# Kernel tuning notes

Measured on AMD Instinct MI355X. Metric: run time of the kernel, lower is better.

The kernel has to match this reference:

```python
import jax, jax.numpy as jnp
import numpy as np
import math

N = 50000   # nodes
E = 800000  # edges
D = 64      # in_feat_dim == out_feat_dim
T = 8       # num node types
R = 8       # num relations
SQRT_DK = math.sqrt(D)


def typed_matmul(x, W, types, num_types):
    """Row-wise x[i] @ W[types[i]] without materializing [E, D, D] gathered weights."""
    out = jnp.zeros((x.shape[0], W.shape[-1]), x.dtype)
    for t in range(num_types):
        out = out + jnp.where((types == t)[:, None], x @ W[t], 0.0)
    return out


def segment_softmax(score, index, num_segments):
    smax = jax.ops.segment_max(score, index, num_segments=num_segments)
    ex = jnp.exp(score - smax[index])
    ssum = jax.ops.segment_sum(ex, index, num_segments=num_segments)
    return ex / (ssum[index] + 1e-16)


def setup_inputs() -> dict:
    key = jax.random.key(0)
    ks = jax.random.split(key, 10)
    h = jax.random.normal(ks[0], (N, D), dtype=jnp.float32)
    adj = jax.random.randint(ks[1], (2, E), 0, N, dtype=jnp.int64)
    edge_type = jax.random.randint(ks[2], (E,), 0, R, dtype=jnp.int64)
    node_type = jax.random.randint(ks[3], (N,), 0, T, dtype=jnp.int64)
    k_weights = jax.random.uniform(ks[4], (T, D, D), dtype=jnp.float32)
    q_weights = jax.random.uniform(ks[5], (T, D, D), dtype=jnp.float32)
    v_weights = jax.random.uniform(ks[6], (T, D, D), dtype=jnp.float32)
    a_weights = jax.random.uniform(ks[7], (T, D, D), dtype=jnp.float32)
    relation_att = jax.random.uniform(ks[8], (R, D, D), dtype=jnp.float32)
    relation_msg = jax.random.uniform(ks[9], (R, D, D), dtype=jnp.float32)
    relation_pri = jnp.ones((R, 1), dtype=jnp.float32)
    skip = jnp.ones((T,), dtype=jnp.float32)
    return {
        "h": h, "adj": adj, "edge_type": edge_type, "node_type": node_type,
        "src_type": 0, "dst_type": 0,
        "k_weights": k_weights, "q_weights": q_weights, "v_weights": v_weights,
        "a_weights": a_weights, "relation_pri": relation_pri,
        "relation_att": relation_att, "relation_msg": relation_msg, "skip": skip,
    }


def reference(h, adj, edge_type, node_type, src_type, dst_type,
              k_weights, q_weights, v_weights, a_weights,
              relation_pri, relation_att, relation_msg, skip):
    src = adj[0]  # _j side (messages come from src)
    dst = adj[1]  # _i side (scatter/softmax index)

    # Node-type-indexed projections (done per node, then gathered per edge --
    # identical math to the per-edge bmm in the original).
    k_node = typed_matmul(h, k_weights, node_type, T)  # [N, D]
    q_node = typed_matmul(h, q_weights, node_type, T)
    v_node = typed_matmul(h, v_weights, node_type, T)

    # Relation-indexed per-edge transforms.
    k = typed_matmul(k_node[src], relation_att, edge_type, R)  # [E, D]
    v = typed_matmul(v_node[src], relation_msg, edge_type, R)  # [E, D]
    q = q_node[dst]                                            # [E, D]

    attn_score = jnp.sum(k * q, axis=1, keepdims=True) * relation_pri[edge_type] / SQRT_DK  # [E, 1]
    alpha = segment_softmax(attn_score, dst, N)  # edge softmax over incoming edges
    rst = v * alpha                              # [E, D]

    agg = jax.ops.segment_sum(rst, dst, num_segments=N)  # [N, D]

    # Update: node-type-indexed output transform scaled by sigmoid(skip[type]).
    trans_out = typed_matmul(agg, a_weights, node_type, T)
    alpha_skip = jax.nn.sigmoid(skip[node_type])
    return trans_out * alpha_skip[:, None]
```

## Files before the change

kernel.cpp:

```cpp
#include <hip/hip_runtime.h>
#include <math.h>

typedef float f32x4 __attribute__((ext_vector_type(4)));
typedef short bf16x8 __attribute__((ext_vector_type(8)));
typedef _Float16 f16x8 __attribute__((ext_vector_type(8)));
typedef _Float16 f16x4 __attribute__((ext_vector_type(4)));

#define D 64
#define TT 8
#define RR 8

#define SCAN_TPB 256
#define SCAN_CH 4
#define SCAN_ELEMS (SCAN_TPB * SCAN_CH)

#define HIST_CH 8
#define SCAT_CH 4
#define SCORE_XB 256
#define V2_XB 64
#define AGG_XB 512

__device__ __forceinline__ float bf2f(unsigned short u) {
    union { unsigned int i; float f; } x;
    x.i = ((unsigned int)u) << 16;
    return x.f;
}
__device__ __forceinline__ unsigned short f2bf(float f) {
    union { float f; unsigned int i; } x;
    x.f = f;
    unsigned int i = x.i;
    unsigned int r = (i + 0x7FFFu + ((i >> 16) & 1u)) >> 16;
    return (unsigned short)r;
}
struct BfPair { short hi; short lo; };
__device__ __forceinline__ BfPair split2(float x) {
    BfPair p;
    unsigned short h = f2bf(x);
    p.hi = (short)h;
    p.lo = (short)f2bf(x - bf2f(h));
    return p;
}
__device__ __forceinline__ void load_A_split(const float* __restrict__ p, bf16x8& ah, bf16x8& al) {
#pragma unroll
    for (int i = 0; i < 8; ++i) {
        BfPair s = split2(p[i]);
        ah[i] = s.hi; al[i] = s.lo;
    }
}
__device__ __forceinline__ void load_B_split(const float* __restrict__ W, int ks, int c, int lane,
                                             bf16x8& bh, bf16x8& bl) {
    int n = lane & 15, q = lane >> 4;
#pragma unroll
    for (int i = 0; i < 8; ++i) {
        BfPair s = split2(W[(ks * 32 + q * 8 + i) * 64 + c * 16 + n]);
        bh[i] = s.hi; bl[i] = s.lo;
    }
}
__device__ __forceinline__ void load_B_split_f16(const float* __restrict__ W, int ks, int c, int lane,
                                                 f16x8& bh, f16x8& bl) {
    int n = lane & 15, q = lane >> 4;
#pragma unroll
    for (int i = 0; i < 8; ++i) {
        float w = W[(ks * 32 + q * 8 + i) * 64 + c * 16 + n];
        _Float16 h = (_Float16)w;
        bh[i] = h;
        bl[i] = (_Float16)(w - (float)h);
    }
}
__device__ __forceinline__ f16x8 load_B_frag_f16(const float* __restrict__ W, int ks, int c, int lane) {
    int n = lane & 15, q = lane >> 4;
    f16x8 r;
#pragma unroll
    for (int i = 0; i < 8; ++i)
        r[i] = (_Float16)W[(ks * 32 + q * 8 + i) * 64 + c * 16 + n];
    return r;
}

#define MFMA16(a, b, c) __builtin_amdgcn_mfma_f32_16x16x32_bf16(a, b, c, 0, 0, 0)
#define MFMAH(a, b, c)  __builtin_amdgcn_mfma_f32_16x16x32_f16(a, b, c, 0, 0, 0)

#define SPLIT_MFMA_BODY(acc, A0h, A0l, A1h, A1l, Bh, Bl)          \
    _Pragma("unroll")                                             \
    for (int c = 0; c < 4; ++c) {                                 \
        acc[c] = MFMA16(A0h, Bh[0][c], acc[c]);                   \
        acc[c] = MFMA16(A0l, Bh[0][c], acc[c]);                   \
        acc[c] = MFMA16(A0h, Bl[0][c], acc[c]);                   \
        acc[c] = MFMA16(A1h, Bh[1][c], acc[c]);                   \
        acc[c] = MFMA16(A1l, Bh[1][c], acc[c]);                   \
        acc[c] = MFMA16(A1h, Bl[1][c], acc[c]);                   \
    }

__global__ void hist_kernel(const int* __restrict__ dst, const int* __restrict__ et,
                            const int* __restrict__ nt,
                            int* __restrict__ deg, int* __restrict__ tcnt, int* __restrict__ rcnt,
                            int* __restrict__ erank, int N, int E) {
    __shared__ int l_r[RR], l_t[TT];
    if (threadIdx.x < RR) l_r[threadIdx.x] = 0;
    if (threadIdx.x < TT) l_t[threadIdx.x] = 0;
    __syncthreads();
    const int stride = gridDim.x * blockDim.x;
    const int tid = blockIdx.x * blockDim.x + threadIdx.x;
#pragma unroll
    for (int i = 0; i < HIST_CH; ++i) {
        int e = tid + i * stride;
        if (e < E) {
            erank[e] = atomicAdd(&deg[dst[e]], 1);
            atomicAdd(&l_r[et[e]], 1);
        }
    }
#pragma unroll
    for (int i = 0; i < HIST_CH; ++i) {
        int n = tid + i * stride;
        if (n < N) atomicAdd(&l_t[nt[n]], 1);
    }
    __syncthreads();
    if (threadIdx.x < RR && l_r[threadIdx.x]) atomicAdd(&rcnt[threadIdx.x], l_r[threadIdx.x]);
    if (threadIdx.x < TT && l_t[threadIdx.x]) atomicAdd(&tcnt[threadIdx.x], l_t[threadIdx.x]);
}

__global__ void scan_sum_kernel(const int* __restrict__ deg, int* __restrict__ bsum, int N) {
    __shared__ int ws[SCAN_TPB / 64];
    int tid = threadIdx.x;
    int base = blockIdx.x * SCAN_ELEMS + tid * SCAN_CH;
    int s = 0;
#pragma unroll
    for (int i = 0; i < SCAN_CH; ++i) {
        int idx = base + i;
        if (idx < N) s += deg[idx];
    }
#pragma unroll
    for (int d = 32; d; d >>= 1) s += __shfl_xor(s, d, 64);
    if ((tid & 63) == 0) ws[tid >> 6] = s;
    __syncthreads();
    if (tid == 0) {
        int t = 0;
#pragma unroll
        for (int i = 0; i < SCAN_TPB / 64; ++i) t += ws[i];
        bsum[blockIdx.x] = t;
    }
}
__global__ void scan_out_kernel(const int* __restrict__ deg, const int* __restrict__ bsum, int nsb,
                                int* __restrict__ off, int N, int Etot,
                                const int* __restrict__ tcnt, int* __restrict__ toff, int* __restrict__ tcur,
                                const int* __restrict__ rcnt, int* __restrict__ roff, int* __restrict__ rcur) {
    __shared__ int ts[SCAN_TPB];
    __shared__ int bb;
    int tid = threadIdx.x;
    if (tid < 64) {
        int v = 0;
        if (nsb <= 64) {
            v = (tid < nsb && tid < blockIdx.x) ? bsum[tid] : 0;
#pragma unroll
            for (int d = 32; d; d >>= 1) v += __shfl_xor(v, d, 64);
        } else if (tid == 0) {
            for (int b = 0; b < blockIdx.x; ++b) v += bsum[b];
        }
        if (tid == 0) bb = v;
    }
    if (blockIdx.x == 0 && tid == 1) {
        int a = 0;
        for (int t = 0; t < TT; ++t) { toff[t] = a; tcur[t] = a; a += tcnt[t]; }
        toff[TT] = a;
        int b2 = 0;
        for (int r = 0; r < RR; ++r) { roff[r] = b2; rcur[r] = b2; b2 += rcnt[r]; }
        roff[RR] = b2;
        off[N] = Etot;
    }
    int base = blockIdx.x * SCAN_ELEMS + tid * SCAN_CH;
    int loc[SCAN_CH];
    int s = 0;
#pragma unroll
    for (int i = 0; i < SCAN_CH; ++i) {
        int idx = base + i;
        int v = (idx < N) ? deg[idx] : 0;
        loc[i] = v; s += v;
    }
    ts[tid] = s;
    __syncthreads();
    for (int sh = 1; sh < SCAN_TPB; sh <<= 1) {
        int v = (tid >= sh) ? ts[tid - sh] : 0;
        __syncthreads();
        ts[tid] += v;
        __syncthreads();
    }
    int run = bb + ((tid > 0) ? ts[tid - 1] : 0);
#pragma unroll
    for (int i = 0; i < SCAN_CH; ++i) {
        int idx = base + i;
        if (idx < N) { off[idx] = run; run += loc[i]; }
    }
}

__global__ void scatter_kernel(const int* __restrict__ src, const int* __restrict__ dst,
                               const int* __restrict__ et, const int* __restrict__ nt,
                               const int* __restrict__ offs, const int* __restrict__ erank,
                               int* __restrict__ tcur, int* __restrict__ rcur,
                               int* __restrict__ rsrc, int* __restrict__ rdst,
                               int* __restrict__ rdpos, int* __restrict__ nidx, int N, int E) {
    __shared__ int l_r[RR], l_t[TT], base_r[RR], base_t[TT];
    if (threadIdx.x < RR) l_r[threadIdx.x] = 0;
    if (threadIdx.x < TT) l_t[threadIdx.x] = 0;
    __syncthreads();
    const int stride = gridDim.x * blockDim.x;
    const int tid = blockIdx.x * blockDim.x + threadIdx.x;
    int s[SCAT_CH], d[SCAT_CH], r[SCAT_CH], rrank[SCAT_CH];
    int t[SCAT_CH], trank[SCAT_CH];
#pragma unroll
    for (int i = 0; i < SCAT_CH; ++i) {
        int e = tid + i * stride;
        if (e < E) {
            s[i] = src[e]; d[i] = dst[e]; r[i] = et[e];
            rrank[i] = atomicAdd(&l_r[r[i]], 1);
        }
        int n = tid + i * stride;
        if (n < N) {
            t[i] = nt[n];
            trank[i] = atomicAdd(&l_t[t[i]], 1);
        }
    }
    __syncthreads();
    if (threadIdx.x < RR)
        base_r[threadIdx.x] = l_r[threadIdx.x] ? atomicAdd(&rcur[threadIdx.x], l_r[threadIdx.x]) : 0;
    if (threadIdx.x < TT)
        base_t[threadIdx.x] = l_t[threadIdx.x] ? atomicAdd(&tcur[threadIdx.x], l_t[threadIdx.x]) : 0;
    __syncthreads();
#pragma unroll
    for (int i = 0; i < SCAT_CH; ++i) {
        int e = tid + i * stride;
        if (e < E) {
            int pos = offs[d[i]] + erank[e];
            int rp = base_r[r[i]] + rrank[i];
            rsrc[rp] = s[i]; rdst[rp] = d[i]; rdpos[rp] = pos;
        }
        int n = tid + i * stride;
        if (n < N) nidx[base_t[t[i]] + trank[i]] = n;
    }
}

__global__ void proj_kernel(const float* __restrict__ h,
                            const float* __restrict__ Wk, const float* __restrict__ Wq,
                            const float* __restrict__ Wv,
                            const int* __restrict__ toff, const int* __restrict__ nidx,
                            _Float16* __restrict__ kh16,
                            _Float16* __restrict__ qout, _Float16* __restrict__ vout) {
    const int t = blockIdx.z, a = blockIdx.y, lane = threadIdx.x;
    const int beg = toff[t], end = toff[t + 1], cnt = end - beg;
    if (cnt <= 0) return;
    const int nstrips = (cnt + 15) >> 4;
    const float* W = (a == 0 ? Wk : (a == 1 ? Wq : Wv)) + (size_t)t * 4096;
    const int m = lane & 15, quad = lane >> 4;

    bf16x8 Bh[2][4], Bl[2][4];
#pragma unroll
    for (int ks = 0; ks < 2; ++ks)
#pragma unroll
        for (int c = 0; c < 4; ++c) load_B_split(W, ks, c, lane, Bh[ks][c], Bl[ks][c]);

    _Float16* out = (a == 0) ? kh16 : (a == 1 ? qout : vout);

    for (int s = blockIdx.x; s < nstrips; s += gridDim.x) {
        int base = beg + s * 16;
        int rA = base + m; if (rA > end - 1) rA = end - 1;
        const float* hp = h + (size_t)nidx[rA] * D;
        bf16x8 A0h, A0l, A1h, A1l;
        load_A_split(hp + quad * 8, A0h, A0l);
        load_A_split(hp + 32 + quad * 8, A1h, A1l);
        f32x4 acc[4];
#pragma unroll
        for (int c = 0; c < 4; ++c) acc[c] = (f32x4){0.f, 0.f, 0.f, 0.f};
        SPLIT_MFMA_BODY(acc, A0h, A0l, A1h, A1l, Bh, Bl)
#pragma unroll
        for (int reg = 0; reg < 4; ++reg) {
            int rr = base + quad * 4 + reg;
            if (rr < end) {
                int nid = nidx[rr];
#pragma unroll
                for (int c = 0; c < 4; ++c)
                    out[(size_t)nid * D + c * 16 + m] = (_Float16)acc[c][reg];
            }
        }
    }
}

__global__ void score_v2_kernel(const int* __restrict__ rsrc, const int* __restrict__ rdst,
                                const int* __restrict__ rdpos, const int* __restrict__ roff,
                                const _Float16* __restrict__ kh16,
                                const _Float16* __restrict__ qn, const float* __restrict__ Aatt,
                                const float* __restrict__ pri, int2* __restrict__ rec,
                                const _Float16* __restrict__ vn, const float* __restrict__ Amsg,
                                _Float16* __restrict__ V2, int N) {
    const int r = blockIdx.y;
    const int lane = threadIdx.x & 63;
    const int wv = threadIdx.x >> 6;
    const int m = lane & 15, quad = lane >> 4;

    if (blockIdx.x >= SCORE_XB) {
        const int g = (blockIdx.x - SCORE_XB) * 4 + wv;
        const int nstrips = (N + 15) >> 4;
        const float* W = Amsg + (size_t)r * 4096;
        f16x8 B[2][4];
#pragma unroll
        for (int ks = 0; ks < 2; ++ks)
#pragma unroll
            for (int c = 0; c < 4; ++c) B[ks][c] = load_B_frag_f16(W, ks, c, lane);

        for (int s = g; s < nstrips; s += V2_XB * 4) {
            int base = s * 16;
            int rA = base + m; if (rA > N - 1) rA = N - 1;
            f16x8 A0 = *(const f16x8*)(vn + (size_t)rA * D + quad * 8);
            f16x8 A1 = *(const f16x8*)(vn + (size_t)rA * D + 32 + quad * 8);
            f32x4 acc[4];
#pragma unroll
            for (int c = 0; c < 4; ++c) acc[c] = (f32x4){0.f, 0.f, 0.f, 0.f};
#pragma unroll
            for (int c = 0; c < 4; ++c) {
                acc[c] = MFMAH(A0, B[0][c], acc[c]);
                acc[c] = MFMAH(A1, B[1][c], acc[c]);
            }
#pragma unroll
            for (int reg = 0; reg < 4; ++reg) {
                int rr = base + quad * 4 + reg;
                if (rr < N) {
#pragma unroll
                    for (int c = 0; c < 4; ++c)
                        V2[((size_t)rr * RR + r) * D + c * 16 + m] = (_Float16)acc[c][reg];
                }
            }
        }
        return;
    }

    const int beg = roff[r], end = roff[r + 1], cnt = end - beg;
    if (cnt <= 0) return;
    const int nstrips = (cnt + 15) >> 4;
    const float scale = pri[r] * 0.125f;
    const float* W = Aatt + (size_t)r * 4096;

    f16x8 Bh[2][4], Bl[2][4];
#pragma unroll
    for (int ks = 0; ks < 2; ++ks)
#pragma unroll
        for (int c = 0; c < 4; ++c) load_B_split_f16(W, ks, c, lane, Bh[ks][c], Bl[ks][c]);

    const int g = blockIdx.x * 4 + wv;
    for (int st = g; st < nstrips; st += SCORE_XB * 4) {
        int base = st * 16;
        int ia = base + m; if (ia > cnt - 1) ia = cnt - 1;
        int s = rsrc[beg + ia];
        const _Float16* kr = kh16 + (size_t)s * D;
        f16x8 A0 = *(const f16x8*)(kr + quad * 8);
        f16x8 A1 = *(const f16x8*)(kr + 32 + quad * 8);
        f32x4 acc[4];
#pragma unroll
        for (int c = 0; c < 4; ++c) acc[c] = (f32x4){0.f, 0.f, 0.f, 0.f};
#pragma unroll
        for (int c = 0; c < 4; ++c) {
            acc[c] = MFMAH(A0, Bh[0][c], acc[c]);
            acc[c] = MFMAH(A0, Bl[0][c], acc[c]);
            acc[c] = MFMAH(A1, Bh[1][c], acc[c]);
            acc[c] = MFMAH(A1, Bl[1][c], acc[c]);
        }

        float p4[4];
#pragma unroll
        for (int reg = 0; reg < 4; ++reg) {
            int ie = base + quad * 4 + reg; if (ie > cnt - 1) ie = cnt - 1;
            const _Float16* qp = qn + (size_t)rdst[beg + ie] * D + m;
            float pr = acc[0][reg] * (float)qp[0] + acc[1][reg] * (float)qp[16]
                     + acc[2][reg] * (float)qp[32] + acc[3][reg] * (float)qp[48];
#pragma unroll
            for (int d = 8; d; d >>= 1) pr += __shfl_xor(pr, d, 64);
            p4[reg] = pr;
        }
        if (m < 4) {
            int idx = base + quad * 4 + m;
            if (idx < cnt) {
                float v = (m == 0) ? p4[0] : (m == 1) ? p4[1] : (m == 2) ? p4[2] : p4[3];
                int sagain = rsrc[beg + idx];
                int2 rc;
                rc.x = __float_as_int(v * scale);
                rc.y = (sagain << 3) | r;
                rec[rdpos[beg + idx]] = rc;
            }
        }
    }
}

__global__ void agg_out_kernel(const int* __restrict__ offs, const int2* __restrict__ rec,
                               const _Float16* __restrict__ V2,
                               const float* __restrict__ Wa, const float* __restrict__ skp,
                               const int* __restrict__ toff, const int* __restrict__ nidx,
                               float* __restrict__ out) {
    const int t = blockIdx.y;
    const int beg = toff[t], end = toff[t + 1], cnt = end - beg;
    if (cnt <= 0) return;
    const int nstrips = (cnt + 15) >> 4;
    const int lane = threadIdx.x & 63;
    const int wv = threadIdx.x >> 6;
    const int quad = lane >> 4, ql = lane & 15;
    const int q16 = wv * 4 + quad;
    const int qb = quad << 4;
    const int m = lane & 15, qd = lane >> 4;
    const float sg = 1.f / (1.f + __expf(-skp[t]));

    __shared__ float As[16][68];

    bf16x8 Bh2[2], Bl2[2];
    const float* W = Wa + (size_t)t * 4096;
#pragma unroll
    for (int ks = 0; ks < 2; ++ks) load_B_split(W, ks, wv, lane, Bh2[ks], Bl2[ks]);

    for (int s = blockIdx.x; s < nstrips; s += gridDim.x) {
        int base = beg + s * 16;
        int rr = base + q16; if (rr > end - 1) rr = end - 1;
        int i = nidx[rr];
        const int ebeg = offs[i], eend = offs[i + 1];
        float mmax = -INFINITY, lsum = 0.f;
        float a0 = 0.f, a1 = 0.f, a2 = 0.f, a3 = 0.f;
        for (int cs = ebeg; cs < eend; cs += 16) {
            int cl = eend - cs; if (cl > 16) cl = 16;
            int2 rc; rc.y = 0;
            float sc = -INFINITY;
            if (ql < cl) { rc = rec[cs + ql]; sc = __int_as_float(rc.x); }
            float cm = sc;
#pragma unroll
            for (int d = 8; d; d >>= 1) cm = fmaxf(cm, __shfl_xor(cm, d, 64));
            float mn = fmaxf(mmax, cm);
            float cf = __expf(mmax - mn);
            float ex = (ql < cl) ? __expf(sc - mn) : 0.f;
            float csum = ex;
#pragma unroll
            for (int d = 8; d; d >>= 1) csum += __shfl_xor(csum, d, 64);
            lsum = lsum * cf + csum;
            a0 *= cf; a1 *= cf; a2 *= cf; a3 *= cf;
            for (int e = 0; e < cl; e += 4) {
                float w0 = __shfl(ex, qb + e, 64),     w1 = __shfl(ex, qb + e + 1, 64);
                float w2 = __shfl(ex, qb + e + 2, 64), w3 = __shfl(ex, qb + e + 3, 64);
                int   i0 = __shfl(rc.y, qb + e, 64),     i1 = __shfl(rc.y, qb + e + 1, 64);
                int   i2 = __shfl(rc.y, qb + e + 2, 64), i3 = __shfl(rc.y, qb + e + 3, 64);
                f16x4 v0 = *(const f16x4*)(V2 + (size_t)i0 * D + ql * 4);
                f16x4 v1 = *(const f16x4*)(V2 + (size_t)i1 * D + ql * 4);
                f16x4 v2 = *(const f16x4*)(V2 + (size_t)i2 * D + ql * 4);
                f16x4 v3 = *(const f16x4*)(V2 + (size_t)i3 * D + ql * 4);
                a0 += w0 * (float)v0[0] + w1 * (float)v1[0] + w2 * (float)v2[0] + w3 * (float)v3[0];
                a1 += w0 * (float)v0[1] + w1 * (float)v1[1] + w2 * (float)v2[1] + w3 * (float)v3[1];
                a2 += w0 * (float)v0[2] + w1 * (float)v1[2] + w2 * (float)v2[2] + w3 * (float)v3[2];
                a3 += w0 * (float)v0[3] + w1 * (float)v1[3] + w2 * (float)v2[3] + w3 * (float)v3[3];
            }
            mmax = mn;
        }
        float inv = 1.f / (lsum + 1e-16f);
        As[q16][ql * 4 + 0] = a0 * inv;
        As[q16][ql * 4 + 1] = a1 * inv;
        As[q16][ql * 4 + 2] = a2 * inv;
        As[q16][ql * 4 + 3] = a3 * inv;
        __syncthreads();

        bf16x8 A0h, A0l, A1h, A1l;
        load_A_split(&As[m][qd * 8], A0h, A0l);
        load_A_split(&As[m][32 + qd * 8], A1h, A1l);
        f32x4 acc = (f32x4){0.f, 0.f, 0.f, 0.f};
        acc = MFMA16(A0h, Bh2[0], acc);
        acc = MFMA16(A0l, Bh2[0], acc);
        acc = MFMA16(A0h, Bl2[0], acc);
        acc = MFMA16(A1h, Bh2[1], acc);
        acc = MFMA16(A1l, Bh2[1], acc);
        acc = MFMA16(A1h, Bl2[1], acc);
#pragma unroll
        for (int reg = 0; reg < 4; ++reg) {
            int rrr = base + qd * 4 + reg;
            if (rrr < end)
                out[(size_t)nidx[rrr] * D + wv * 16 + m] = acc[reg] * sg;
        }
        __syncthreads();
    }
}

extern "C" void kernel_launch(void* const* d_in, const int* in_sizes, int n_in,
                              void* d_out, int out_size, void* d_ws, size_t ws_size,
                              hipStream_t stream) {
    const float* h     = (const float*)d_in[0];
    const int*   adj   = (const int*)d_in[1];
    const int*   etype = (const int*)d_in[2];
    const int*   ntype = (const int*)d_in[3];
    const float* Wk    = (const float*)d_in[6];
    const float* Wq    = (const float*)d_in[7];
    const float* Wv    = (const float*)d_in[8];
    const float* Wa    = (const float*)d_in[9];
    const float* pri   = (const float*)d_in[10];
    const float* Aatt  = (const float*)d_in[11];
    const float* Amsg  = (const float*)d_in[12];
    const float* skp   = (const float*)d_in[13];
    const int N = in_sizes[3];
    const int E = in_sizes[2];
    float* out = (float*)d_out;

    char* w = (char*)d_ws;
    auto alloc = [&](size_t b) { char* p = w; w += (b + 255) & ~(size_t)255; return p; };
    _Float16* kh16 = (_Float16*)alloc((size_t)N * D * 2);
    _Float16* qn   = (_Float16*)alloc((size_t)N * D * 2);
    _Float16* vn   = (_Float16*)alloc((size_t)N * D * 2);
    _Float16* V2   = (_Float16*)alloc((size_t)N * RR * D * 2);
    int* deg  = (int*)alloc((size_t)(N + 16) * 4);
    int* tcnt = deg + N;
    int* rcnt = deg + N + 8;
    int* offs = (int*)alloc((size_t)(N + 1) * 4);
    int* erank = (int*)alloc((size_t)E * 4);
    int* toff = (int*)alloc(64);
    int* tcur = (int*)alloc(64);
    int* roff = (int*)alloc(64);
    int* rcur = (int*)alloc(64);
    int2* rec = (int2*)alloc((size_t)E * 8);
    int* rsrc  = (int*)alloc((size_t)E * 4);
    int* rdst  = (int*)alloc((size_t)E * 4);
    int* rdpos = (int*)alloc((size_t)E * 4);
    int* nidx  = (int*)alloc((size_t)N * 4);
    const int nsb = (N + SCAN_ELEMS - 1) / SCAN_ELEMS;
    int* bsum  = (int*)alloc((size_t)nsb * 4);

    (void)hipMemsetAsync(deg, 0, (size_t)(N + 16) * 4, stream);

    const int mx = (E > N ? E : N);
    const int histBlocks = (mx + 256 * HIST_CH - 1) / (256 * HIST_CH);
    hist_kernel<<<histBlocks, 256, 0, stream>>>(adj + E, etype, ntype, deg, tcnt, rcnt, erank, N, E);
    scan_sum_kernel<<<nsb, SCAN_TPB, 0, stream>>>(deg, bsum, N);
    scan_out_kernel<<<nsb, SCAN_TPB, 0, stream>>>(deg, bsum, nsb, offs, N, E,
                                                  tcnt, toff, tcur, rcnt, roff, rcur);
    const int scatBlocks = (mx + 256 * SCAT_CH - 1) / (256 * SCAT_CH);
    scatter_kernel<<<scatBlocks, 256, 0, stream>>>(adj, adj + E, etype, ntype,
                                                   offs, erank, tcur, rcur,
                                                   rsrc, rdst, rdpos, nidx, N, E);
    proj_kernel<<<dim3(128, 3, TT), 64, 0, stream>>>(h, Wk, Wq, Wv, toff, nidx, kh16, qn, vn);
    score_v2_kernel<<<dim3(SCORE_XB + V2_XB, RR), 256, 0, stream>>>(rsrc, rdst, rdpos, roff,
                                                                    kh16, qn, Aatt, pri, rec,
                                                                    vn, Amsg, V2, N);
    agg_out_kernel<<<dim3(AGG_XB, TT), 256, 0, stream>>>(offs, rec, V2, Wa, skp, toff, nidx, out);
}
```

Measured before the change: 258.0 us.

## Fuse CSR build stages into one cooperative kernel with grid syncs

Replaces the memset, histogram, two scan kernels and scatter kernel with a single cooperative build kernel that separates the phases with grid-wide syncs. Per-edge data (packed src/relation, dst, rank) stays in registers between phases, so the erank buffer and the re-reads of src, dst and edge type go away. This is meant to cut several launch gaps and some global traffic, at the cost of four grid barriers. The kernel also assumes the fixed grid covers all edges (8 per thread) and all nodes (one per thread), so it only works for sizes within that limit.

```diff
diff --git a/kernel.cpp b/kernel.cpp
--- a/kernel.cpp
+++ b/kernel.cpp
@@ -1,5 +1,8 @@
 #include <hip/hip_runtime.h>
+#include <hip/hip_cooperative_groups.h>
 #include <math.h>
+
+namespace cg = cooperative_groups;
 
 typedef float f32x4 __attribute__((ext_vector_type(4)));
 typedef short bf16x8 __attribute__((ext_vector_type(8)));
@@ -14,8 +17,8 @@
 #define SCAN_CH 4
 #define SCAN_ELEMS (SCAN_TPB * SCAN_CH)
 
-#define HIST_CH 8
-#define SCAT_CH 4
+#define BUILD_XB 512
+#define BUILD_EPT 8
 #define SCORE_XB 256
 #define V2_XB 64
 #define AGG_XB 512
@@ -90,151 +93,141 @@
         acc[c] = MFMA16(A1h, Bl[1][c], acc[c]);                   \
     }
 
-__global__ void hist_kernel(const int* __restrict__ dst, const int* __restrict__ et,
-                            const int* __restrict__ nt,
-                            int* __restrict__ deg, int* __restrict__ tcnt, int* __restrict__ rcnt,
-                            int* __restrict__ erank, int N, int E) {
-    __shared__ int l_r[RR], l_t[TT];
+__global__ void build_kernel(const int* __restrict__ src, const int* __restrict__ dst,
+                             const int* __restrict__ et, const int* __restrict__ nt,
+                             int* __restrict__ deg,
+                             int* __restrict__ offs,
+                             int* __restrict__ toff, int* __restrict__ tcur,
+                             int* __restrict__ roff, int* __restrict__ rcur,
+                             int* __restrict__ rsrc, int* __restrict__ rdst,
+                             int* __restrict__ rdpos, int* __restrict__ nidx,
+                             int* __restrict__ bsum, int nsb, int N, int E) {
+    cg::grid_group grid = cg::this_grid();
+    const int tid = blockIdx.x * blockDim.x + threadIdx.x;
+    const int nth = gridDim.x * blockDim.x;
+    int* tcnt = deg + N;
+    int* rcnt = deg + N + 8;
+
+    __shared__ int l_r[RR], l_t[TT], base_r[RR], base_t[TT];
+    __shared__ int ts[SCAN_TPB];
+    __shared__ int ws[SCAN_TPB / 64];
+    __shared__ int bbs;
+
+    for (int i = tid; i < N + 16; i += nth) deg[i] = 0;
     if (threadIdx.x < RR) l_r[threadIdx.x] = 0;
     if (threadIdx.x < TT) l_t[threadIdx.x] = 0;
-    __syncthreads();
-    const int stride = gridDim.x * blockDim.x;
-    const int tid = blockIdx.x * blockDim.x + threadIdx.x;
-#pragma unroll
-    for (int i = 0; i < HIST_CH; ++i) {
-        int e = tid + i * stride;
+    grid.sync();
+
+    int epk[BUILD_EPT], ed[BUILD_EPT], erk[BUILD_EPT], rrk[BUILD_EPT];
+#pragma unroll
+    for (int i = 0; i < BUILD_EPT; ++i) {
+        int e = tid + i * nth;
         if (e < E) {
-            erank[e] = atomicAdd(&deg[dst[e]], 1);
-            atomicAdd(&l_r[et[e]], 1);
-        }
-    }
-#pragma unroll
-    for (int i = 0; i < HIST_CH; ++i) {
-        int n = tid + i * stride;
-        if (n < N) atomicAdd(&l_t[nt[n]], 1);
+            int s = src[e], d = dst[e], r = et[e];
+            epk[i] = (s << 3) | r;
+            ed[i] = d;
+            erk[i] = atomicAdd(&deg[d], 1);
+            rrk[i] = atomicAdd(&l_r[r], 1);
+        }
+    }
+    int myt = 0, mytrank = 0;
+    if (tid < N) {
+        myt = nt[tid];
+        mytrank = atomicAdd(&l_t[myt], 1);
     }
     __syncthreads();
     if (threadIdx.x < RR && l_r[threadIdx.x]) atomicAdd(&rcnt[threadIdx.x], l_r[threadIdx.x]);
     if (threadIdx.x < TT && l_t[threadIdx.x]) atomicAdd(&tcnt[threadIdx.x], l_t[threadIdx.x]);
-}
-
-__global__ void scan_sum_kernel(const int* __restrict__ deg, int* __restrict__ bsum, int N) {
-    __shared__ int ws[SCAN_TPB / 64];
-    int tid = threadIdx.x;
-    int base = blockIdx.x * SCAN_ELEMS + tid * SCAN_CH;
-    int s = 0;
-#pragma unroll
-    for (int i = 0; i < SCAN_CH; ++i) {
-        int idx = base + i;
-        if (idx < N) s += deg[idx];
-    }
-#pragma unroll
-    for (int d = 32; d; d >>= 1) s += __shfl_xor(s, d, 64);
-    if ((tid & 63) == 0) ws[tid >> 6] = s;
-    __syncthreads();
-    if (tid == 0) {
-        int t = 0;
-#pragma unroll
-        for (int i = 0; i < SCAN_TPB / 64; ++i) t += ws[i];
-        bsum[blockIdx.x] = t;
-    }
-}
-__global__ void scan_out_kernel(const int* __restrict__ deg, const int* __restrict__ bsum, int nsb,
-                                int* __restrict__ off, int N, int Etot,
-                                const int* __restrict__ tcnt, int* __restrict__ toff, int* __restrict__ tcur,
-                                const int* __restrict__ rcnt, int* __restrict__ roff, int* __restrict__ rcur) {
-    __shared__ int ts[SCAN_TPB];
-    __shared__ int bb;
-    int tid = threadIdx.x;
-    if (tid < 64) {
-        int v = 0;
-        if (nsb <= 64) {
-            v = (tid < nsb && tid < blockIdx.x) ? bsum[tid] : 0;
-#pragma unroll
-            for (int d = 32; d; d >>= 1) v += __shfl_xor(v, d, 64);
-        } else if (tid == 0) {
-            for (int b = 0; b < blockIdx.x; ++b) v += bsum[b];
-        }
-        if (tid == 0) bb = v;
-    }
-    if (blockIdx.x == 0 && tid == 1) {
-        int a = 0;
-        for (int t = 0; t < TT; ++t) { toff[t] = a; tcur[t] = a; a += tcnt[t]; }
-        toff[TT] = a;
-        int b2 = 0;
-        for (int r = 0; r < RR; ++r) { roff[r] = b2; rcur[r] = b2; b2 += rcnt[r]; }
-        roff[RR] = b2;
-        off[N] = Etot;
-    }
-    int base = blockIdx.x * SCAN_ELEMS + tid * SCAN_CH;
-    int loc[SCAN_CH];
-    int s = 0;
-#pragma unroll
-    for (int i = 0; i < SCAN_CH; ++i) {
-        int idx = base + i;
-        int v = (idx < N) ? deg[idx] : 0;
-        loc[i] = v; s += v;
-    }
-    ts[tid] = s;
-    __syncthreads();
-    for (int sh = 1; sh < SCAN_TPB; sh <<= 1) {
-        int v = (tid >= sh) ? ts[tid - sh] : 0;
+    grid.sync();
+
+    if (blockIdx.x < nsb) {
+        int t0 = threadIdx.x;
+        int base = blockIdx.x * SCAN_ELEMS + t0 * SCAN_CH;
+        int s = 0;
+#pragma unroll
+        for (int i = 0; i < SCAN_CH; ++i) {
+            int idx = base + i;
+            if (idx < N) s += deg[idx];
+        }
+#pragma unroll
+        for (int d = 32; d; d >>= 1) s += __shfl_xor(s, d, 64);
+        if ((t0 & 63) == 0) ws[t0 >> 6] = s;
         __syncthreads();
-        ts[tid] += v;
+        if (t0 == 0) {
+            int t = 0;
+#pragma unroll
+            for (int i = 0; i < SCAN_TPB / 64; ++i) t += ws[i];
+            bsum[blockIdx.x] = t;
+        }
+    }
+    grid.sync();
+
+    if (blockIdx.x < nsb) {
+        int t0 = threadIdx.x;
+        if (t0 < 64) {
+            int v = 0;
+            if (nsb <= 64) {
+                v = (t0 < nsb && t0 < blockIdx.x) ? bsum[t0] : 0;
+#pragma unroll
+                for (int d = 32; d; d >>= 1) v += __shfl_xor(v, d, 64);
+            } else if (t0 == 0) {
+                for (int b = 0; b < blockIdx.x; ++b) v += bsum[b];
+            }
+            if (t0 == 0) bbs = v;
+        }
+        if (blockIdx.x == 0 && t0 == 1) {
+            int a = 0;
+            for (int t = 0; t < TT; ++t) { toff[t] = a; tcur[t] = a; a += tcnt[t]; }
+            toff[TT] = a;
+            int b2 = 0;
+            for (int r = 0; r < RR; ++r) { roff[r] = b2; rcur[r] = b2; b2 += rcnt[r]; }
+            roff[RR] = b2;
+            offs[N] = E;
+        }
+        int base = blockIdx.x * SCAN_ELEMS + t0 * SCAN_CH;
+        int loc[SCAN_CH];
+        int s = 0;
+#pragma unroll
+        for (int i = 0; i < SCAN_CH; ++i) {
+            int idx = base + i;
+            int v = (idx < N) ? deg[idx] : 0;
+            loc[i] = v; s += v;
+        }
+        ts[t0] = s;
         __syncthreads();
-    }
-    int run = bb + ((tid > 0) ? ts[tid - 1] : 0);
-#pragma unroll
-    for (int i = 0; i < SCAN_CH; ++i) {
-        int idx = base + i;
-        if (idx < N) { off[idx] = run; run += loc[i]; }
-    }
-}
-
-__global__ void scatter_kernel(const int* __restrict__ src, const int* __restrict__ dst,
-                               const int* __restrict__ et, const int* __restrict__ nt,
-                               const int* __restrict__ offs, const int* __restrict__ erank,
-                               int* __restrict__ tcur, int* __restrict__ rcur,
-                               int* __restrict__ rsrc, int* __restrict__ rdst,
-                               int* __restrict__ rdpos, int* __restrict__ nidx, int N, int E) {
-    __shared__ int l_r[RR], l_t[TT], base_r[RR], base_t[TT];
-    if (threadIdx.x < RR) l_r[threadIdx.x] = 0;
-    if (threadIdx.x < TT) l_t[threadIdx.x] = 0;
-    __syncthreads();
-    const int stride = gridDim.x * blockDim.x;
-    const int tid = blockIdx.x * blockDim.x + threadIdx.x;
-    int s[SCAT_CH], d[SCAT_CH], r[SCAT_CH], rrank[SCAT_CH];
-    int t[SCAT_CH], trank[SCAT_CH];
-#pragma unroll
-    for (int i = 0; i < SCAT_CH; ++i) {
-        int e = tid + i * stride;
-        if (e < E) {
-            s[i] = src[e]; d[i] = dst[e]; r[i] = et[e];
-            rrank[i] = atomicAdd(&l_r[r[i]], 1);
-        }
-        int n = tid + i * stride;
-        if (n < N) {
-            t[i] = nt[n];
-            trank[i] = atomicAdd(&l_t[t[i]], 1);
-        }
-    }
-    __syncthreads();
+        for (int sh = 1; sh < SCAN_TPB; sh <<= 1) {
+            int v = (t0 >= sh) ? ts[t0 - sh] : 0;
+            __syncthreads();
+            ts[t0] += v;
+            __syncthreads();
+        }
+        int run = bbs + ((t0 > 0) ? ts[t0 - 1] : 0);
+#pragma unroll
+        for (int i = 0; i < SCAN_CH; ++i) {
+            int idx = base + i;
+            if (idx < N) { offs[idx] = run; run += loc[i]; }
+        }
+    }
+    grid.sync();
+
     if (threadIdx.x < RR)
         base_r[threadIdx.x] = l_r[threadIdx.x] ? atomicAdd(&rcur[threadIdx.x], l_r[threadIdx.x]) : 0;
     if (threadIdx.x < TT)
         base_t[threadIdx.x] = l_t[threadIdx.x] ? atomicAdd(&tcur[threadIdx.x], l_t[threadIdx.x]) : 0;
     __syncthreads();
 #pragma unroll
-    for (int i = 0; i < SCAT_CH; ++i) {
-        int e = tid + i * stride;
+    for (int i = 0; i < BUILD_EPT; ++i) {
+        int e = tid + i * nth;
         if (e < E) {
-            int pos = offs[d[i]] + erank[e];
-            int rp = base_r[r[i]] + rrank[i];
-            rsrc[rp] = s[i]; rdst[rp] = d[i]; rdpos[rp] = pos;
-        }
-        int n = tid + i * stride;
-        if (n < N) nidx[base_t[t[i]] + trank[i]] = n;
-    }
+            int r = epk[i] & 7;
+            int pos = offs[ed[i]] + erk[i];
+            int rp = base_r[r] + rrk[i];
+            rsrc[rp] = epk[i] >> 3;
+            rdst[rp] = ed[i];
+            rdpos[rp] = pos;
+        }
+    }
+    if (tid < N) nidx[base_t[myt] + mytrank] = tid;
 }
 
 __global__ void proj_kernel(const float* __restrict__ h,
@@ -502,10 +495,7 @@
     _Float16* vn   = (_Float16*)alloc((size_t)N * D * 2);
     _Float16* V2   = (_Float16*)alloc((size_t)N * RR * D * 2);
     int* deg  = (int*)alloc((size_t)(N + 16) * 4);
-    int* tcnt = deg + N;
-    int* rcnt = deg + N + 8;
     int* offs = (int*)alloc((size_t)(N + 1) * 4);
-    int* erank = (int*)alloc((size_t)E * 4);
     int* toff = (int*)alloc(64);
     int* tcur = (int*)alloc(64);
     int* roff = (int*)alloc(64);
@@ -518,18 +508,19 @@
     const int nsb = (N + SCAN_ELEMS - 1) / SCAN_ELEMS;
     int* bsum  = (int*)alloc((size_t)nsb * 4);
 
-    (void)hipMemsetAsync(deg, 0, (size_t)(N + 16) * 4, stream);
-
-    const int mx = (E > N ? E : N);
-    const int histBlocks = (mx + 256 * HIST_CH - 1) / (256 * HIST_CH);
-    hist_kernel<<<histBlocks, 256, 0, stream>>>(adj + E, etype, ntype, deg, tcnt, rcnt, erank, N, E);
-    scan_sum_kernel<<<nsb, SCAN_TPB, 0, stream>>>(deg, bsum, N);
-    scan_out_kernel<<<nsb, SCAN_TPB, 0, stream>>>(deg, bsum, nsb, offs, N, E,
-                                                  tcnt, toff, tcur, rcnt, roff, rcur);
-    const int scatBlocks = (mx + 256 * SCAT_CH - 1) / (256 * SCAT_CH);
-    scatter_kernel<<<scatBlocks, 256, 0, stream>>>(adj, adj + E, etype, ntype,
-                                                   offs, erank, tcur, rcur,
-                                                   rsrc, rdst, rdpos, nidx, N, E);
+    const int* srcp = adj;
+    const int* dstp = adj + E;
+    int nsb_v = nsb, N_v = N, E_v = E;
+    void* args[] = {
+        (void*)&srcp, (void*)&dstp, (void*)&etype, (void*)&ntype,
+        (void*)&deg, (void*)&offs,
+        (void*)&toff, (void*)&tcur, (void*)&roff, (void*)&rcur,
+        (void*)&rsrc, (void*)&rdst, (void*)&rdpos, (void*)&nidx,
+        (void*)&bsum, (void*)&nsb_v, (void*)&N_v, (void*)&E_v,
+    };
+    (void)hipLaunchCooperativeKernel((void*)build_kernel, dim3(BUILD_XB), dim3(256),
+                                     args, 0, stream);
+
     proj_kernel<<<dim3(128, 3, TT), 64, 0, stream>>>(h, Wk, Wq, Wv, toff, nidx, kh16, qn, vn);
     score_v2_kernel<<<dim3(SCORE_XB + V2_XB, RR), 256, 0, stream>>>(rsrc, rdst, rdpos, roff,
                                                                     kh16, qn, Aatt, pri, rec,
```

New measurement: 462.9 us. 1.79x slower.
